# Optimization experiments

Hardware: AMD Instinct MI355X
Metric: run time of the kernel (lower is better)

## Reference

```python
import jax, jax.numpy as jnp
import numpy as np

IN_FEATURES = 1024
OUT_FEATURES = 1024
GRID_SIZE = 5
SPLINE_ORDER = 3
GRID_RANGE = (-1.0, 1.0)


def make_grid():
    h = (GRID_RANGE[1] - GRID_RANGE[0]) / GRID_SIZE
    g = jnp.arange(-SPLINE_ORDER, GRID_SIZE + SPLINE_ORDER + 1, dtype=jnp.float32) * h + GRID_RANGE[0]
    return jnp.tile(g[None, :], (IN_FEATURES, 1))  # (in, G + 2k + 1)


def b_splines(x, grid):
    # x: (N, in), grid: (in, G+2k+1) -> bases: (N, in, G+k)
    xe = x[..., None]
    bases = ((xe >= grid[:, :-1]) & (xe < grid[:, 1:])).astype(x.dtype)
    for k in range(1, SPLINE_ORDER + 1):
        left = (xe - grid[:, :-(k + 1)]) / (grid[:, k:-1] - grid[:, :-(k + 1)])
        right = (grid[:, k + 1:] - xe) / (grid[:, k + 1:] - grid[:, 1:-k])
        bases = left * bases[:, :, :-1] + right * bases[:, :, 1:]
    return bases


def setup_inputs() -> dict:
    key = jax.random.key(0)
    k1, k2, k3 = jax.random.split(key, 3)
    x = jax.random.uniform(k1, (8192, IN_FEATURES), dtype=jnp.float32)
    # lecun_normal-style init: std = 1/sqrt(fan_in)
    base_weight = jax.random.normal(k2, (OUT_FEATURES, IN_FEATURES), dtype=jnp.float32) / np.sqrt(IN_FEATURES)
    coeff = GRID_SIZE + SPLINE_ORDER
    spline_weight = jax.random.normal(k3, (OUT_FEATURES, IN_FEATURES, coeff), dtype=jnp.float32) / np.sqrt(IN_FEATURES * coeff)
    spline_scaler = jnp.ones((OUT_FEATURES, IN_FEATURES), dtype=jnp.float32)
    grid = make_grid()
    return {"x": x, "grid": grid, "base_weight": base_weight,
            "spline_weight": spline_weight, "spline_scaler": spline_scaler}


def reference(x, grid, base_weight, spline_weight, spline_scaler):
    N = x.shape[0]
    base_out = jax.nn.silu(x) @ base_weight.T  # (N, out)
    bases = b_splines(x, grid)                 # (N, in, G+k)
    scaled_sw = spline_weight * spline_scaler[..., None]  # (out, in, G+k)
    spline_out = bases.reshape(N, -1) @ scaled_sw.reshape(OUT_FEATURES, -1).T  # (N, out)
    return base_out + spline_out
```

## Files before the change

kernel.cpp:

```cpp
#include <hip/hip_runtime.h>
#include <hip/hip_bf16.h>

#define IN_F 1024
#define OUT_F 1024
#define KTOT (IN_F * 9)
#define M_ROWS 8192

#define BM 256
#define BN 128
#define BK 64
#define NT (KTOT / BK)

typedef short bf16x8 __attribute__((ext_vector_type(8)));
typedef int   i32x4  __attribute__((ext_vector_type(4)));
typedef float f32x4  __attribute__((ext_vector_type(4)));

#define AS1 __attribute__((address_space(1)))
#define AS3 __attribute__((address_space(3)))

__device__ __forceinline__ void kan_basis_fast(
    float xv, const float* __restrict__ g,
    const float* __restrict__ inv1, const float* __restrict__ inv2,
    const float* __restrict__ inv3, float* __restrict__ out) {
  float b[11];
#pragma unroll
  for (int j = 0; j < 11; ++j)
    b[j] = (xv >= g[j] && xv < g[j + 1]) ? 1.0f : 0.0f;
#pragma unroll
  for (int j = 0; j < 10; ++j)
    b[j] = (xv - g[j]) * inv1[j] * b[j] + (g[j + 2] - xv) * inv1[j + 1] * b[j + 1];
#pragma unroll
  for (int j = 0; j < 9; ++j)
    b[j] = (xv - g[j]) * inv2[j] * b[j] + (g[j + 3] - xv) * inv2[j + 1] * b[j + 1];
#pragma unroll
  for (int j = 0; j < 8; ++j)
    b[j] = (xv - g[j]) * inv3[j] * b[j] + (g[j + 4] - xv) * inv3[j + 1] * b[j + 1];
#pragma unroll
  for (int j = 0; j < 8; ++j) out[j] = b[j];
}

__global__ __launch_bounds__(256) void expand_a(
    const float* __restrict__ x, const float* __restrict__ grid,
    __hip_bfloat16* __restrict__ A, int row0, int nrows) {
  const int tid = threadIdx.x;
  const int lane = tid & 63;
  const int wvx = tid >> 6;
  const int l15 = lane & 15;
  const int lhi = lane >> 4;

  const int nb = blockIdx.x >> 3;
  const int ib = blockIdx.x & 7;
  const int n_l = nb * 16 + l15;
  const int i0 = ib * 128 + wvx * 32 + lhi * 8;

  const int bm = n_l >> 8, wm = (n_l >> 6) & 3, m = (n_l >> 4) & 3;

  float g[12];
  const float* gp = grid + (size_t)i0 * 12;
#pragma unroll
  for (int j = 0; j < 12; ++j) g[j] = gp[j];
  float inv1[11], inv2[10], inv3[9];
#pragma unroll
  for (int j = 0; j < 11; ++j) inv1[j] = 1.0f / (g[j + 1] - g[j]);
#pragma unroll
  for (int j = 0; j < 10; ++j) inv2[j] = 1.0f / (g[j + 2] - g[j]);
#pragma unroll
  for (int j = 0; j < 9; ++j)  inv3[j] = 1.0f / (g[j + 3] - g[j]);

  const float* xp = x + (size_t)(row0 + n_l) * IN_F + i0;
  float xs[8];
  *(f32x4*)&xs[0] = *(const f32x4*)xp;
  *(f32x4*)&xs[4] = *(const f32x4*)(xp + 4);

  bf16x8 out[9];
#pragma unroll
  for (int j = 0; j < 8; ++j) {
    float xv = xs[j];
    float bas[8];
    kan_basis_fast(xv, g, inv1, inv2, inv3, bas);
    float s = xv / (1.0f + __expf(-xv));
    out[0][j] = (short)__bfloat16_as_ushort(__float2bfloat16(s));
#pragma unroll
    for (int c = 0; c < 8; ++c)
      out[c + 1][j] = (short)__bfloat16_as_ushort(__float2bfloat16(bas[c]));
  }

#pragma unroll
  for (int c = 0; c < 9; ++c) {
    int k0 = c * IN_F + i0;
    int kt = k0 >> 6;
    int kk = (k0 >> 5) & 1;
    size_t frag = ((((size_t)bm * NT + kt) * 4 + wm) * 4 + m) * 2 + kk;
    *(bf16x8*)(A + frag * 512 + lane * 8) = out[c];
  }
}

__global__ __launch_bounds__(256) void pack_b(
    const float* __restrict__ bw, const float* __restrict__ sw,
    const float* __restrict__ sc, __hip_bfloat16* __restrict__ B) {
  int t = blockIdx.x * 256 + threadIdx.x;
  if (t >= OUT_F * 128) return;
  int o = t >> 7;
  int i0 = (t & 127) * 8;

  float bwv[8], scv[8];
  const float* bp = bw + (size_t)o * IN_F + i0;
  const float* sp = sc + (size_t)o * IN_F + i0;
  *(f32x4*)&bwv[0] = *(const f32x4*)bp;
  *(f32x4*)&bwv[4] = *(const f32x4*)(bp + 4);
  *(f32x4*)&scv[0] = *(const f32x4*)sp;
  *(f32x4*)&scv[4] = *(const f32x4*)(sp + 4);

  bf16x8 out[9];
#pragma unroll
  for (int j = 0; j < 8; ++j) {
    out[0][j] = (short)__bfloat16_as_ushort(__float2bfloat16(bwv[j]));
    const float* swp = sw + ((size_t)o * IN_F + i0 + j) * 8;
    float swv[8];
    *(f32x4*)&swv[0] = *(const f32x4*)swp;
    *(f32x4*)&swv[4] = *(const f32x4*)(swp + 4);
#pragma unroll
    for (int c = 0; c < 8; ++c)
      out[c + 1][j] = (short)__bfloat16_as_ushort(__float2bfloat16(swv[c] * scv[j]));
  }
  __hip_bfloat16* dst = B + (size_t)o * KTOT + i0;
#pragma unroll
  for (int c = 0; c < 9; ++c)
    *(bf16x8*)(dst + (size_t)c * IN_F) = out[c];
}


__device__ __forceinline__ void gld16(const __hip_bfloat16* g, __hip_bfloat16* l) {
  __builtin_amdgcn_global_load_lds((AS1 void*)g, (AS3 void*)l, 16, 0, 0);
}

__device__ __forceinline__ bf16x8 dsr128(uint32_t addr) {
  i32x4 r;
  asm volatile("ds_read_b128 %0, %1" : "=v"(r) : "v"(addr));
  return __builtin_bit_cast(bf16x8, r);
}

#define SB __builtin_amdgcn_sched_barrier(0)

#define READ_B(dB, slot, h) do {                                           \
    uint32_t bS_ = bBase + (uint32_t)(slot) * (BN * BK * 2);               \
    _Pragma("unroll")                                                      \
    for (int n_ = 0; n_ < 4; ++n_) dB[n_] = dsr128(bS_ + bOffB[h][n_]);    \
  } while (0)

#define A_LOAD(DST) do {                                                   \
    _Pragma("unroll")                                                      \
    for (int m_ = 0; m_ < 4; ++m_) {                                       \
      DST[m_][0] = *(const bf16x8*)(aTile + m_ * 1024);                    \
      DST[m_][1] = *(const bf16x8*)(aTile + m_ * 1024 + 512);              \
    }                                                                      \
    aTile += 16384;                                                        \
  } while (0)

#define MFMA_K(CUR, H, BFR) do {                                           \
    __builtin_amdgcn_s_setprio(1);                                         \
    _Pragma("unroll")                                                      \
    for (int m_ = 0; m_ < 4; ++m_)                                         \
      _Pragma("unroll")                                                    \
      for (int n_ = 0; n_ < 4; ++n_)                                       \
        acc[m_][n_] = __builtin_amdgcn_mfma_f32_16x16x32_bf16(             \
            CUR[m_][H], BFR[n_], acc[m_][n_], 0, 0, 0);                    \
    __builtin_amdgcn_s_setprio(0);                                         \
  } while (0)

#define STAGE_B(slot, koff) do {                                           \
    __hip_bfloat16* bsD_ = &Bs[slot][0];                                   \
    gld16(bSrc[0] + (koff), bsD_ + bDst[0]);                               \
    gld16(bSrc[1] + (koff), bsD_ + bDst[1]);                               \
  } while (0)

#define TILE_FULL(CUR, NXT, KT2) do {                                      \
    const int nxt_ = cur == 2 ? 0 : cur + 1;                               \
    const int stg_ = cur == 0 ? 2 : cur - 1;                               \
    READ_B(gb, cur, 1);                             \
    STAGE_B(stg_, KT2);                                                    \
    A_LOAD(NXT);                                                           \
    SB;                                                                    \
    asm volatile("s_waitcnt lgkmcnt(4)" ::: "memory"); SB;                 \
    MFMA_K(CUR, 0, fb);        \
    SB;                                                                    \
    asm volatile("s_waitcnt lgkmcnt(0)" ::: "memory"); SB;                 \
    asm volatile("s_waitcnt vmcnt(10)" ::: "memory"); SB;                  \
    __builtin_amdgcn_s_barrier(); SB;              \
    READ_B(fb, nxt_, 0);                                                   \
    SB;                                                                    \
    MFMA_K(CUR, 1, gb);                                                    \
    SB;                                                                    \
    cur = nxt_;                                                            \
  } while (0)

#define TILE_NT2(CUR, NXT) do {                                            \
    const int nxt_ = cur == 2 ? 0 : cur + 1;                               \
    READ_B(gb, cur, 1);                                                    \
    A_LOAD(NXT);                                                           \
    SB;                                                                    \
    asm volatile("s_waitcnt lgkmcnt(4)" ::: "memory"); SB;                 \
    MFMA_K(CUR, 0, fb);                                                    \
    SB;                                                                    \
    asm volatile("s_waitcnt lgkmcnt(0)" ::: "memory"); SB;                 \
    asm volatile("s_waitcnt vmcnt(8)" ::: "memory"); SB;                   \
    __builtin_amdgcn_s_barrier(); SB;                                      \
    READ_B(fb, nxt_, 0);                                                   \
    SB;                                                                    \
    MFMA_K(CUR, 1, gb);                                                    \
    SB;                                                                    \
    cur = nxt_;                                                            \
  } while (0)

#define TILE_LAST(CUR) do {                                                \
    READ_B(gb, cur, 1);                                                    \
    SB;                                                                    \
    asm volatile("s_waitcnt lgkmcnt(4)" ::: "memory"); SB;                 \
    MFMA_K(CUR, 0, fb);                                                    \
    SB;                                                                    \
    asm volatile("s_waitcnt lgkmcnt(0)" ::: "memory"); SB;                 \
    MFMA_K(CUR, 1, gb);                                                    \
    SB;                                                                    \
  } while (0)

__global__ __launch_bounds__(512, 2) void gemm_v9(
    const __hip_bfloat16* __restrict__ A, const __hip_bfloat16* __restrict__ B,
    float* __restrict__ C) {
  __shared__ __align__(16) __hip_bfloat16 Bs[3][BN * BK];

  const int nwg = gridDim.x;
  const int q = nwg >> 3;
  const int L = (blockIdx.x & 7) * q + (blockIdx.x >> 3);
  const int bm = L >> 3, bn = L & 7;

  const int tid = threadIdx.x;
  const int lane = tid & 63;
  const int wv = tid >> 6;
  const int wm = wv >> 1;
  const int wn = wv & 1;
  const int l15 = lane & 15, lhi = lane >> 4;
  const int K = KTOT;

  const __hip_bfloat16* bSrc[2];
  int bDst[2];
#pragma unroll
  for (int j = 0; j < 2; ++j) {
    int p = j * 512 + wv * 64 + lane;
    int row = p >> 3;
    int col = (p & 7) ^ (row & 7);
    bSrc[j] = B + (size_t)(bn * BN + row) * K + col * 8;
    bDst[j] = (j * 512 + wv * 64) * 8;
  }

  const uint32_t bBase = (uint32_t)(uintptr_t)(AS3 const void*)&Bs[0][0];
  uint32_t bOffB[2][4];
#pragma unroll
  for (int h = 0; h < 2; ++h)
#pragma unroll
    for (int n = 0; n < 4; ++n) {
      int rowB = wn * 64 + n * 16 + l15;
      bOffB[h][n] = (rowB * 64 + (((h * 4 + lhi) ^ (l15 & 7)) * 8)) * 2;
    }

  const __hip_bfloat16* aTile =
      A + (size_t)bm * NT * 16384 + wm * 4096 + lane * 8;

  f32x4 acc[4][4];
#pragma unroll
  for (int m = 0; m < 4; ++m)
#pragma unroll
    for (int n = 0; n < 4; ++n) acc[m][n] = f32x4{0.f, 0.f, 0.f, 0.f};

  bf16x8 faA[4][2], faB[4][2];
  bf16x8 fb[4], gb[4];

  STAGE_B(0, 0);
  STAGE_B(1, BK);
  A_LOAD(faA);
  asm volatile("s_waitcnt vmcnt(10)" ::: "memory");
  SB;
  __builtin_amdgcn_s_barrier();
  SB;
  READ_B(fb, 0, 0);
  SB;

  int cur = 0;
  int kt2 = 2 * BK;
#pragma unroll 1
  for (int tt = 0; tt < (NT - 2) / 2; ++tt) {
    TILE_FULL(faA, faB, kt2); kt2 += BK;
    TILE_FULL(faB, faA, kt2); kt2 += BK;
  }
  TILE_NT2(faA, faB);
  TILE_LAST(faB);

#pragma unroll
  for (int m = 0; m < 4; ++m)
#pragma unroll
    for (int n = 0; n < 4; ++n) {
      int col = bn * BN + wn * 64 + n * 16 + l15;
      int row0 = bm * BM + wm * 64 + m * 16 + lhi * 4;
#pragma unroll
      for (int j = 0; j < 4; ++j)
        C[(size_t)(row0 + j) * OUT_F + col] = acc[m][n][j];
    }
}

__global__ __launch_bounds__(256) void kan_naive(
    const float* __restrict__ x, const float* __restrict__ grid,
    const float* __restrict__ bw, const float* __restrict__ sw,
    const float* __restrict__ sc, float* __restrict__ out) {
  __shared__ float s_act[IN_F];
  __shared__ float s_bas[IN_F * 8];
  int n = blockIdx.x;
  for (int i = threadIdx.x; i < IN_F; i += 256) {
    float xv = x[(size_t)n * IN_F + i];
    float g[12];
    const float* gp = grid + i * 12;
#pragma unroll
    for (int t = 0; t < 12; ++t) g[t] = gp[t];
    float b[11];
#pragma unroll
    for (int j = 0; j < 11; ++j)
      b[j] = (xv >= g[j] && xv < g[j + 1]) ? 1.0f : 0.0f;
#pragma unroll
    for (int k = 1; k <= 3; ++k)
#pragma unroll
      for (int j = 0; j < 11 - k; ++j) {
        float left = (xv - g[j]) / (g[j + k] - g[j]);
        float right = (g[j + k + 1] - xv) / (g[j + k + 1] - g[j + 1]);
        b[j] = left * b[j] + right * b[j + 1];
      }
    s_act[i] = xv / (1.0f + __expf(-xv));
#pragma unroll
    for (int c = 0; c < 8; ++c) s_bas[i * 8 + c] = b[c];
  }
  __syncthreads();
  for (int o = threadIdx.x; o < OUT_F; o += 256) {
    float acc = 0.f;
    const float* bwo = bw + (size_t)o * IN_F;
    const float* swo = sw + (size_t)o * IN_F * 8;
    const float* sco = sc + (size_t)o * IN_F;
    for (int i = 0; i < IN_F; ++i) {
      acc += s_act[i] * bwo[i];
      float p = 0.f;
#pragma unroll
      for (int c = 0; c < 8; ++c) p += s_bas[i * 8 + c] * swo[i * 8 + c];
      acc += p * sco[i];
    }
    out[(size_t)n * OUT_F + o] = acc;
  }
}

extern "C" void kernel_launch(void* const* d_in, const int* in_sizes, int n_in,
                              void* d_out, int out_size, void* d_ws, size_t ws_size,
                              hipStream_t stream) {
  const float* x  = (const float*)d_in[0];
  const float* grid = (const float*)d_in[1];
  const float* bw = (const float*)d_in[2];
  const float* sw = (const float*)d_in[3];
  const float* sc = (const float*)d_in[4];
  float* out = (float*)d_out;

  const size_t Bbytes = (size_t)OUT_F * KTOT * 2;
  const size_t rowBytes = (size_t)KTOT * 2;

  if (ws_size >= Bbytes + 256 * rowBytes) {
    __hip_bfloat16* Bp = (__hip_bfloat16*)d_ws;
    __hip_bfloat16* Ap = (__hip_bfloat16*)((char*)d_ws + Bbytes);
    size_t arows = (ws_size - Bbytes) / rowBytes;
    int chunk = (int)((arows / 256) * 256);
    if (chunk > M_ROWS) chunk = M_ROWS;

    pack_b<<<OUT_F * 128 / 256, 256, 0, stream>>>(bw, sw, sc, Bp);
    for (int r0 = 0; r0 < M_ROWS; r0 += chunk) {
      int rows = M_ROWS - r0 < chunk ? M_ROWS - r0 : chunk;
      expand_a<<<(rows / 16) * 8, 256, 0, stream>>>(x, grid, Ap, r0, rows);
      gemm_v9<<<(rows / BM) * 8, 512, 0, stream>>>(Ap, Bp, out + (size_t)r0 * OUT_F);
    }
  } else {
    kan_naive<<<M_ROWS, 256, 0, stream>>>(x, grid, bw, sw, sc, out);
  }
}
```

Measured before the change: 218.6 us.

## Stage A and B tiles through LDS with fragment-packed B layout

B is now packed into MFMA fragment order so it matches the A layout, and the GEMM stages both A and B tiles into a triple-buffered LDS ring using direct global-to-LDS loads. A was previously loaded from global straight into registers. Both operands are then read from LDS with conflict-free linear offsets. This is meant to cut register pressure and global-load latency on the A path and to remove the XOR swizzle, at the cost of a larger LDS footprint per block (about 144 KB for three slots), which may limit how many blocks fit on each CU.

```diff
diff --git a/kernel.cpp b/kernel.cpp
--- a/kernel.cpp
+++ b/kernel.cpp
@@ -10,6 +10,9 @@
 #define BN 128
 #define BK 64
 #define NT (KTOT / BK)
+
+#define A_TILE_E 16384
+#define B_TILE_E 8192
 
 typedef short bf16x8 __attribute__((ext_vector_type(8)));
 typedef int   i32x4  __attribute__((ext_vector_type(4)));
@@ -98,10 +101,15 @@
 __global__ __launch_bounds__(256) void pack_b(
     const float* __restrict__ bw, const float* __restrict__ sw,
     const float* __restrict__ sc, __hip_bfloat16* __restrict__ B) {
-  int t = blockIdx.x * 256 + threadIdx.x;
-  if (t >= OUT_F * 128) return;
-  int o = t >> 7;
-  int i0 = (t & 127) * 8;
+  const int tid = threadIdx.x;
+  const int lane = tid & 63;
+  const int wid = blockIdx.x * 4 + (tid >> 6);
+  const int og = wid >> 5;
+  const int ib32 = wid & 31;
+  const int bn = og >> 3, colg = og & 7;
+  const int l15 = lane & 15, lhi = lane >> 4;
+  const int o = og * 16 + l15;
+  const int i0 = ib32 * 32 + lhi * 8;
 
   float bwv[8], scv[8];
   const float* bp = bw + (size_t)o * IN_F + i0;
@@ -123,10 +131,14 @@
     for (int c = 0; c < 8; ++c)
       out[c + 1][j] = (short)__bfloat16_as_ushort(__float2bfloat16(swv[c] * scv[j]));
   }
-  __hip_bfloat16* dst = B + (size_t)o * KTOT + i0;
-#pragma unroll
-  for (int c = 0; c < 9; ++c)
-    *(bf16x8*)(dst + (size_t)c * IN_F) = out[c];
+
+#pragma unroll
+  for (int c = 0; c < 9; ++c) {
+    int kt = c * 16 + (ib32 >> 1);
+    int kk = ib32 & 1;
+    size_t frag = ((size_t)bn * NT + kt) * 16 + colg * 2 + kk;
+    *(bf16x8*)(B + frag * 512 + lane * 8) = out[c];
+  }
 }
 
 
@@ -142,91 +154,91 @@
 
 #define SB __builtin_amdgcn_sched_barrier(0)
 
-#define READ_B(dB, slot, h) do {                                           \
-    uint32_t bS_ = bBase + (uint32_t)(slot) * (BN * BK * 2);               \
+#define SLOT_B 49152
+#define SLOT_E 24576
+
+#define READ_FRAGS(dA, dB, slot, h) do {                                   \
+    uint32_t s_ = ldsB + (uint32_t)(slot) * SLOT_B;                        \
     _Pragma("unroll")                                                      \
-    for (int n_ = 0; n_ < 4; ++n_) dB[n_] = dsr128(bS_ + bOffB[h][n_]);    \
-  } while (0)
-
-#define A_LOAD(DST) do {                                                   \
+    for (int m_ = 0; m_ < 4; ++m_) dA[m_] = dsr128(s_ + aOff[h][m_]);      \
     _Pragma("unroll")                                                      \
-    for (int m_ = 0; m_ < 4; ++m_) {                                       \
-      DST[m_][0] = *(const bf16x8*)(aTile + m_ * 1024);                    \
-      DST[m_][1] = *(const bf16x8*)(aTile + m_ * 1024 + 512);              \
-    }                                                                      \
-    aTile += 16384;                                                        \
-  } while (0)
-
-#define MFMA_K(CUR, H, BFR) do {                                           \
+    for (int n_ = 0; n_ < 4; ++n_) dB[n_] = dsr128(s_ + bOff[h][n_]);      \
+  } while (0)
+
+#define MFMA_BURST(sA, sB) do {                                            \
     __builtin_amdgcn_s_setprio(1);                                         \
     _Pragma("unroll")                                                      \
     for (int m_ = 0; m_ < 4; ++m_)                                         \
       _Pragma("unroll")                                                    \
       for (int n_ = 0; n_ < 4; ++n_)                                       \
         acc[m_][n_] = __builtin_amdgcn_mfma_f32_16x16x32_bf16(             \
-            CUR[m_][H], BFR[n_], acc[m_][n_], 0, 0, 0);                    \
+            sA[m_], sB[n_], acc[m_][n_], 0, 0, 0);                         \
     __builtin_amdgcn_s_setprio(0);                                         \
   } while (0)
 
-#define STAGE_B(slot, koff) do {                                           \
-    __hip_bfloat16* bsD_ = &Bs[slot][0];                                   \
-    gld16(bSrc[0] + (koff), bsD_ + bDst[0]);                               \
-    gld16(bSrc[1] + (koff), bsD_ + bDst[1]);                               \
-  } while (0)
-
-#define TILE_FULL(CUR, NXT, KT2) do {                                      \
+#define STAGE_T(slot, t) do {                                              \
+    __hip_bfloat16* d_ = ldsP + (slot) * SLOT_E;                           \
+    const __hip_bfloat16* aT_ = aG + (size_t)(t) * A_TILE_E;               \
+    const __hip_bfloat16* bT_ = bG + (size_t)(t) * B_TILE_E;               \
+    gld16(aT_,         d_ + dstE);                                         \
+    gld16(aT_ + 4096,  d_ + dstE + 4096);                                  \
+    gld16(aT_ + 8192,  d_ + dstE + 8192);                                  \
+    gld16(aT_ + 12288, d_ + dstE + 12288);                                 \
+    gld16(bT_,         d_ + 16384 + dstE);                                 \
+    gld16(bT_ + 4096,  d_ + 16384 + dstE + 4096);                          \
+  } while (0)
+
+#define TILE_FULL(t) do {                                                  \
     const int nxt_ = cur == 2 ? 0 : cur + 1;                               \
     const int stg_ = cur == 0 ? 2 : cur - 1;                               \
-    READ_B(gb, cur, 1);                             \
-    STAGE_B(stg_, KT2);                                                    \
-    A_LOAD(NXT);                                                           \
-    SB;                                                                    \
-    asm volatile("s_waitcnt lgkmcnt(4)" ::: "memory"); SB;                 \
-    MFMA_K(CUR, 0, fb);        \
+    READ_FRAGS(ga, gb, cur, 1);                               \
+    STAGE_T(stg_, (t) + 2);                                  \
+    SB;                                                                    \
+    asm volatile("s_waitcnt lgkmcnt(8)" ::: "memory"); SB;                 \
+    MFMA_BURST(fa, fb);                                                    \
     SB;                                                                    \
     asm volatile("s_waitcnt lgkmcnt(0)" ::: "memory"); SB;                 \
-    asm volatile("s_waitcnt vmcnt(10)" ::: "memory"); SB;                  \
-    __builtin_amdgcn_s_barrier(); SB;              \
-    READ_B(fb, nxt_, 0);                                                   \
-    SB;                                                                    \
-    MFMA_K(CUR, 1, gb);                                                    \
+    asm volatile("s_waitcnt vmcnt(6)" ::: "memory"); SB;                   \
+    __builtin_amdgcn_s_barrier(); SB;                     \
+    READ_FRAGS(fa, fb, nxt_, 0);                               \
+    SB;                                                                    \
+    MFMA_BURST(ga, gb);                                                    \
     SB;                                                                    \
     cur = nxt_;                                                            \
   } while (0)
 
-#define TILE_NT2(CUR, NXT) do {                                            \
+#define TILE_NT2() do {                                                    \
     const int nxt_ = cur == 2 ? 0 : cur + 1;                               \
-    READ_B(gb, cur, 1);                                                    \
-    A_LOAD(NXT);                                                           \
-    SB;                                                                    \
-    asm volatile("s_waitcnt lgkmcnt(4)" ::: "memory"); SB;                 \
-    MFMA_K(CUR, 0, fb);                                                    \
+    READ_FRAGS(ga, gb, cur, 1);                                            \
+    SB;                                                                    \
+    asm volatile("s_waitcnt lgkmcnt(8)" ::: "memory"); SB;                 \
+    MFMA_BURST(fa, fb);                                                    \
     SB;                                                                    \
     asm volatile("s_waitcnt lgkmcnt(0)" ::: "memory"); SB;                 \
-    asm volatile("s_waitcnt vmcnt(8)" ::: "memory"); SB;                   \
+    asm volatile("s_waitcnt vmcnt(0)" ::: "memory"); SB;                   \
     __builtin_amdgcn_s_barrier(); SB;                                      \
-    READ_B(fb, nxt_, 0);                                                   \
-    SB;                                                                    \
-    MFMA_K(CUR, 1, gb);                                                    \
+    READ_FRAGS(fa, fb, nxt_, 0);                                           \
+    SB;                                                                    \
+    MFMA_BURST(ga, gb);                                                    \
     SB;                                                                    \
     cur = nxt_;                                                            \
   } while (0)
 
-#define TILE_LAST(CUR) do {                                                \
-    READ_B(gb, cur, 1);                                                    \
-    SB;                                                                    \
-    asm volatile("s_waitcnt lgkmcnt(4)" ::: "memory"); SB;                 \
-    MFMA_K(CUR, 0, fb);                                                    \
+#define TILE_LAST() do {                                                   \
+    READ_FRAGS(ga, gb, cur, 1);                                            \
+    SB;                                                                    \
+    asm volatile("s_waitcnt lgkmcnt(8)" ::: "memory"); SB;                 \
+    MFMA_BURST(fa, fb);                                                    \
     SB;                                                                    \
     asm volatile("s_waitcnt lgkmcnt(0)" ::: "memory"); SB;                 \
-    MFMA_K(CUR, 1, gb);                                                    \
-    SB;                                                                    \
-  } while (0)
-
-__global__ __launch_bounds__(512, 2) void gemm_v9(
+    MFMA_BURST(ga, gb);                                                    \
+    SB;                                                                    \
+  } while (0)
+
+__global__ __launch_bounds__(512, 2) void gemm_v11(
     const __hip_bfloat16* __restrict__ A, const __hip_bfloat16* __restrict__ B,
     float* __restrict__ C) {
-  __shared__ __align__(16) __hip_bfloat16 Bs[3][BN * BK];
+  __shared__ __align__(16) __hip_bfloat16 S[3][SLOT_E];
 
   const int nwg = gridDim.x;
   const int q = nwg >> 3;
@@ -239,60 +251,44 @@
   const int wm = wv >> 1;
   const int wn = wv & 1;
   const int l15 = lane & 15, lhi = lane >> 4;
-  const int K = KTOT;
-
-  const __hip_bfloat16* bSrc[2];
-  int bDst[2];
-#pragma unroll
-  for (int j = 0; j < 2; ++j) {
-    int p = j * 512 + wv * 64 + lane;
-    int row = p >> 3;
-    int col = (p & 7) ^ (row & 7);
-    bSrc[j] = B + (size_t)(bn * BN + row) * K + col * 8;
-    bDst[j] = (j * 512 + wv * 64) * 8;
-  }
-
-  const uint32_t bBase = (uint32_t)(uintptr_t)(AS3 const void*)&Bs[0][0];
-  uint32_t bOffB[2][4];
+
+  const __hip_bfloat16* aG = A + (size_t)bm * NT * A_TILE_E + (wv * 64 + lane) * 8;
+  const __hip_bfloat16* bG = B + (size_t)bn * NT * B_TILE_E + (wv * 64 + lane) * 8;
+  __hip_bfloat16* ldsP = &S[0][0];
+  const int dstE = wv * 512;
+
+  const uint32_t ldsB = (uint32_t)(uintptr_t)(AS3 const void*)&S[0][0];
+  uint32_t aOff[2][4], bOff[2][4];
 #pragma unroll
   for (int h = 0; h < 2; ++h)
 #pragma unroll
-    for (int n = 0; n < 4; ++n) {
-      int rowB = wn * 64 + n * 16 + l15;
-      bOffB[h][n] = (rowB * 64 + (((h * 4 + lhi) ^ (l15 & 7)) * 8)) * 2;
+    for (int m = 0; m < 4; ++m) {
+      aOff[h][m] = (uint32_t)((wm * 8 + m * 2 + h) * 1024 + lane * 16);
+      bOff[h][m] = (uint32_t)(32768 + ((wn * 4 + m) * 2 + h) * 1024 + lane * 16);
     }
 
-  const __hip_bfloat16* aTile =
-      A + (size_t)bm * NT * 16384 + wm * 4096 + lane * 8;
-
   f32x4 acc[4][4];
 #pragma unroll
   for (int m = 0; m < 4; ++m)
 #pragma unroll
     for (int n = 0; n < 4; ++n) acc[m][n] = f32x4{0.f, 0.f, 0.f, 0.f};
 
-  bf16x8 faA[4][2], faB[4][2];
-  bf16x8 fb[4], gb[4];
-
-  STAGE_B(0, 0);
-  STAGE_B(1, BK);
-  A_LOAD(faA);
-  asm volatile("s_waitcnt vmcnt(10)" ::: "memory");
+  bf16x8 fa[4], fb[4];
+  bf16x8 ga[4], gb[4];
+
+  STAGE_T(0, 0);
+  STAGE_T(1, 1);
+  asm volatile("s_waitcnt vmcnt(6)" ::: "memory");
   SB;
   __builtin_amdgcn_s_barrier();
   SB;
-  READ_B(fb, 0, 0);
+  READ_FRAGS(fa, fb, 0, 0);
   SB;
 
   int cur = 0;
-  int kt2 = 2 * BK;
-#pragma unroll 1
-  for (int tt = 0; tt < (NT - 2) / 2; ++tt) {
-    TILE_FULL(faA, faB, kt2); kt2 += BK;
-    TILE_FULL(faB, faA, kt2); kt2 += BK;
-  }
-  TILE_NT2(faA, faB);
-  TILE_LAST(faB);
+  for (int t = 0; t < NT - 2; ++t) TILE_FULL(t);
+  TILE_NT2();
+  TILE_LAST();
 
 #pragma unroll
   for (int m = 0; m < 4; ++m)
@@ -376,7 +372,7 @@
     for (int r0 = 0; r0 < M_ROWS; r0 += chunk) {
       int rows = M_ROWS - r0 < chunk ? M_ROWS - r0 : chunk;
       expand_a<<<(rows / 16) * 8, 256, 0, stream>>>(x, grid, Ap, r0, rows);
-      gemm_v9<<<(rows / BM) * 8, 512, 0, stream>>>(Ap, Bp, out + (size_t)r0 * OUT_F);
+      gemm_v11<<<(rows / BM) * 8, 512, 0, stream>>>(Ap, Bp, out + (size_t)r0 * OUT_F);
     }
   } else {
     kan_naive<<<M_ROWS, 256, 0, stream>>>(x, grid, bw, sw, sc, out);
```

Measured after the change: 183.4 us. 1.19x faster.
